# Optimization experiments

Hardware: AMD Instinct MI355X
Metric: run time of the kernel (lower is better)

The kernel has to match this reference:

```python
import jax, jax.numpy as jnp
import numpy as np
from jax import lax

PAD = 1
T, B, V, E, H, K = 256, 64, 50000, 300, 256, 20  # H = hidden_dim//2 per direction


def setup_inputs() -> dict:
    key = jax.random.key(0)
    ks = jax.random.split(key, 14)
    lengths = jnp.sort(jax.random.randint(ks[0], (B,), T // 2, T + 1))[::-1]  # sorted desc like pack_padded
    toks = jax.random.randint(ks[1], (T, B), 2, V)
    tpos = jnp.arange(T)[:, None]
    x = jnp.where(tpos < lengths[None, :], toks, PAD)
    n = jax.random.normal
    s = 1.0 / np.sqrt(H)
    emb = (n(ks[2], (V, E)) * 0.1).at[PAD].set(0.0)  # padding_idx row zeroed
    Wih0 = n(ks[3], (2, 4 * H, E)) * s       # [dir, 4H, in]
    Whh0 = n(ks[4], (2, 4 * H, H)) * s
    b0 = n(ks[5], (2, 4 * H)) * s            # b_ih + b_hh folded together
    Wih1 = n(ks[6], (2, 4 * H, 2 * H)) * s
    Whh1 = n(ks[7], (2, 4 * H, H)) * s
    b1 = n(ks[8], (2, 4 * H)) * s
    W_out = n(ks[9], (K, 2 * H)) * s
    b_out = n(ks[10], (K,)) * s
    trans = n(ks[11], (K, K)) * 0.1
    start = n(ks[12], (K,)) * 0.1
    end = n(ks[13], (K,)) * 0.1
    return dict(x=x, sent_lengths=lengths, emb=emb, Wih0=Wih0, Whh0=Whh0, b0=b0,
                Wih1=Wih1, Whh1=Whh1, b1=b1, W_out=W_out, b_out=b_out,
                trans=trans, start=start, end=end)


def _lstm_dir(xs, m, Wih, Whh, b):
    # xs [T,B,D], m [T,B,1] float mask. PyTorch gate order i,f,g,o.
    xg = jnp.einsum('tbd,gd->tbg', xs, Wih) + b  # big GEMM up-front
    h0 = jnp.zeros((xs.shape[1], H), xs.dtype)

    def step(carry, inp):
        h, c = carry
        g_t, m_t = inp
        gates = g_t + h @ Whh.T
        i, f, g, o = jnp.split(gates, 4, -1)
        c_new = jax.nn.sigmoid(f) * c + jax.nn.sigmoid(i) * jnp.tanh(g)
        h_new = jax.nn.sigmoid(o) * jnp.tanh(c_new)
        # freeze state at padded steps (pack_padded semantics); padded outputs are zero
        return (jnp.where(m_t > 0, h_new, h), jnp.where(m_t > 0, c_new, c)), h_new * m_t

    _, out = lax.scan(step, (h0, h0), (xg, m))
    return out


def _bilstm(xs, m, rev, Wih, Whh, b):
    out_f = _lstm_dir(xs, m, Wih[0], Whh[0], b[0])
    xs_r = jnp.take_along_axis(xs, rev[:, :, None], 0)  # reverse within each length
    out_b = jnp.take_along_axis(_lstm_dir(xs_r, m, Wih[1], Whh[1], b[1]), rev[:, :, None], 0)
    return jnp.concatenate([out_f, out_b], -1)


def reference(x, sent_lengths, emb, Wih0, Whh0, b0, Wih1, Whh1, b1, W_out, b_out, trans, start, end):
    mask = x != PAD                               # [T,B]
    m = mask[:, :, None].astype(emb.dtype)
    tpos = jnp.arange(T)[:, None]
    rev = jnp.where(tpos < sent_lengths[None, :], sent_lengths[None, :] - 1 - tpos, tpos)
    h = emb[x]                                    # [T,B,E]
    h = _bilstm(h, m, rev, Wih0, Whh0, b0)
    h = _bilstm(h, m, rev, Wih1, Whh1, b1)
    emis = jnp.einsum('tbh,kh->tbk', h, W_out) + b_out  # [T,B,K]

    # Viterbi decode (torchcrf semantics)
    score0 = start[None, :] + emis[0]             # [B,K]

    def vstep(sc, inp):
        e_t, m_t = inp
        cand = sc[:, :, None] + trans[None] + e_t[:, None, :]  # [B,prev,next]
        best = cand.max(1)
        ptr = cand.argmax(1).astype(jnp.int32)
        sc2 = jnp.where(m_t[:, None], best, sc)
        # identity pointer at padded steps so backtrace passes tags through
        ptr = jnp.where(m_t[:, None], ptr, jnp.arange(K, dtype=jnp.int32)[None, :])
        return sc2, ptr

    score, hist = lax.scan(vstep, score0, (emis[1:], mask[1:]))
    score = score + end[None, :]                  # score frozen at seq end -> same as adding at last valid step
    last = jnp.argmax(score, -1).astype(jnp.int32)

    def back(tag, ptr):
        prev = jnp.take_along_axis(ptr, tag[:, None], 1)[:, 0]
        return prev, prev

    _, tags_prev = lax.scan(back, last, hist, reverse=True)
    tags = jnp.concatenate([tags_prev, last[None, :]], 0)  # [T,B]
    return jnp.where(mask, tags, 0)
```

## Files before the change

### kernel.cpp

```cpp
#include <hip/hip_runtime.h>
#include <stdint.h>


#define T_ 256
#define B_ 64
#define EPAD 304
#define KTAG 20
#define TB_ (T_ * B_)
#define RES 80
#define NQ 44


__global__ void prep_embed(const int* __restrict__ x, const float* __restrict__ emb,
                           float* __restrict__ xsA) {
  int r = blockIdx.x;
  int tok = x[r];
  const float* src = emb + (size_t)tok * 300;
  for (int e = threadIdx.x; e < EPAD; e += 64)
    xsA[(size_t)r * EPAD + e] = (e < 300) ? src[e] : 0.f;
}

__global__ void prep_b0t(const float* __restrict__ Wih0, float* __restrict__ B0t) {
  int idx = blockIdx.x * 256 + threadIdx.x;
  if (idx >= 2048 * EPAD) return;
  int n = idx / EPAD, k = idx % EPAD;
  B0t[idx] = (k < 300) ? Wih0[(size_t)n * 300 + k] : 0.f;
}

__global__ void prep_bot64(const float* __restrict__ Wout, float* __restrict__ Bot,
                           const float* __restrict__ bout, float* __restrict__ biaso) {
  int idx = blockIdx.x * 256 + threadIdx.x;
  int n = idx >> 9, k = idx & 511;
  Bot[idx] = (n < KTAG) ? Wout[(size_t)n * 512 + k] : 0.f;
  if (idx < 64) biaso[idx] = (idx < KTAG) ? bout[idx] : 0.f;
}

__global__ void prep_whh2(const float* __restrict__ Whh, float* __restrict__ whhL) {
  int idx = blockIdx.x * 256 + threadIdx.x;
  int d = idx >> 18, rem = idx & 262143, k = rem >> 10, tg = rem & 1023;
  int row = (tg & 3) * 256 + (tg >> 2);
  float v = Whh[(size_t)d * 262144 + (size_t)row * 256 + k];
  if (k < RES) whhL[(size_t)(d * RES + k) * 1024 + tg] = v;
  else {
    int kk = k - RES, q = kk >> 2, e = kk & 3;
    whhL[(size_t)2 * RES * 1024 + ((size_t)(d * NQ + q) * 1024 + tg) * 4 + e] = v;
  }
}

__global__ __launch_bounds__(256) void gemm_f32(
    const float* __restrict__ A, int lda, const float* __restrict__ Bt, int ldb,
    float* __restrict__ C, int ldc, const float* __restrict__ bias,
    int ntn, int K) {
  const int tm = blockIdx.x / ntn, tn = blockIdx.x % ntn;
  const int m0 = tm * 64, n0 = tn * 64;
  __shared__ __align__(16) float As[16][64];
  __shared__ __align__(16) float Bs[16][64];
  const int tid = threadIdx.x;
  const int mm = tid >> 2, kq = (tid & 3) * 4;
  const int tx = tid & 15, ty = tid >> 4;
  float acc[4][4] = {};
  for (int k0 = 0; k0 < K; k0 += 16) {
    float4 av = *(const float4*)&A[(size_t)(m0 + mm) * lda + k0 + kq];
    float4 bv = *(const float4*)&Bt[(size_t)(n0 + mm) * ldb + k0 + kq];
    __syncthreads();
    As[kq + 0][mm] = av.x; As[kq + 1][mm] = av.y;
    As[kq + 2][mm] = av.z; As[kq + 3][mm] = av.w;
    Bs[kq + 0][mm] = bv.x; Bs[kq + 1][mm] = bv.y;
    Bs[kq + 2][mm] = bv.z; Bs[kq + 3][mm] = bv.w;
    __syncthreads();
#pragma unroll
    for (int kk = 0; kk < 16; ++kk) {
      float4 a4 = *(const float4*)&As[kk][ty * 4];
      float4 b4 = *(const float4*)&Bs[kk][tx * 4];
      acc[0][0] += a4.x * b4.x; acc[0][1] += a4.x * b4.y;
      acc[0][2] += a4.x * b4.z; acc[0][3] += a4.x * b4.w;
      acc[1][0] += a4.y * b4.x; acc[1][1] += a4.y * b4.y;
      acc[1][2] += a4.y * b4.z; acc[1][3] += a4.y * b4.w;
      acc[2][0] += a4.z * b4.x; acc[2][1] += a4.z * b4.y;
      acc[2][2] += a4.z * b4.z; acc[2][3] += a4.z * b4.w;
      acc[3][0] += a4.w * b4.x; acc[3][1] += a4.w * b4.y;
      acc[3][2] += a4.w * b4.z; acc[3][3] += a4.w * b4.w;
    }
  }
#pragma unroll
  for (int i = 0; i < 4; ++i)
#pragma unroll
    for (int j = 0; j < 4; ++j)
      C[(size_t)(m0 + ty * 4 + i) * ldc + n0 + tx * 4 + j] =
          acc[i][j] + bias[n0 + tx * 4 + j];
}

__global__ __launch_bounds__(1024) void lstm_rec(
    const float* __restrict__ xg, const float* __restrict__ whhL,
    float* __restrict__ out, const int* __restrict__ lens) {
  const int wg = blockIdx.x, dir = wg & 1, b = wg >> 1;
  const int len = lens[b];
  const int tg = threadIdx.x;
  const int j = tg >> 2, gt = tg & 3;
  const int xrow = gt * 256 + j;

  float wres[RES];
#pragma unroll
  for (int p = 0; p < RES; ++p)
    wres[p] = whhL[(size_t)(dir * RES + p) * 1024 + tg];
  const float* sp = whhL + (size_t)2 * RES * 1024 + ((size_t)dir * NQ * 1024 + tg) * 4;

  __shared__ __align__(16) float hsd[2][256];
  if (tg < 256) hsd[0][tg] = 0.f;
  float c = 0.f;
  __syncthreads();

  const int lane = tg & 63, qb = lane & ~3;

  for (int s = 0; s < len; ++s) {
    const int t = dir ? (len - 1 - s) : s;
    const int r = t * B_ + b;
    float xv = xg[(size_t)r * 2048 + dir * 1024 + xrow];
    const float4* Hr = (const float4*)hsd[s & 1];
    float a = 0.f;
#pragma unroll
    for (int p = 0; p < RES / 4; ++p) {
      float4 h4 = Hr[p];
      a += wres[4 * p] * h4.x + wres[4 * p + 1] * h4.y +
           wres[4 * p + 2] * h4.z + wres[4 * p + 3] * h4.w;
    }
#pragma unroll 4
    for (int q = 0; q < NQ; ++q) {
      float4 wv = *(const float4*)(sp + (size_t)q * 4096);
      float4 h4 = Hr[RES / 4 + q];
      a += wv.x * h4.x + wv.y * h4.y + wv.z * h4.z + wv.w * h4.w;
    }
    a += xv;
    float v1 = __shfl(a, qb | 1);
    float v2 = __shfl(a, qb | 2);
    float v3 = __shfl(a, qb | 3);
    if (gt == 0) {
      float si = 1.f / (1.f + expf(-a));
      float sf = 1.f / (1.f + expf(-v1));
      float so = 1.f / (1.f + expf(-v3));
      c = sf * c + si * tanhf(v2);
      float h = so * tanhf(c);
      hsd[(s + 1) & 1][j] = h;
      out[(size_t)r * 512 + dir * 256 + j] = h;
    }
    __syncthreads();
  }
  for (int t = len; t < T_; ++t)
    if (gt == 0) out[(size_t)(t * B_ + b) * 512 + dir * 256 + j] = 0.f;
}

__global__ __launch_bounds__(64) void viterbi(
    const float* __restrict__ emis, const float* __restrict__ trans,
    const float* __restrict__ startv, const float* __restrict__ endv,
    const int* __restrict__ lens, int* __restrict__ outp) {
  int b = blockIdx.x, lane = threadIdx.x;
  __shared__ float tr[KTAG * KTAG];
  __shared__ float fin[KTAG];
  __shared__ unsigned char hist[T_ * KTAG];
  for (int i = lane; i < KTAG * KTAG; i += 64) tr[i] = trans[i];
  int len = lens[b];
  float score = (lane < KTAG) ? startv[lane] + emis[(size_t)b * 64 + lane] : -3e38f;
  __syncthreads();
  for (int t = 1; t < len; ++t) {
    float e = (lane < KTAG) ? emis[(size_t)(t * B_ + b) * 64 + lane] : 0.f;
    float best = -3e38f; int bp = 0;
    for (int p = 0; p < KTAG; ++p) {
      float cand = (__shfl(score, p) + tr[p * KTAG + lane]) + e;
      if (cand > best) { best = cand; bp = p; }
    }
    if (lane < KTAG) { score = best; hist[t * KTAG + lane] = (unsigned char)bp; }
  }
  if (lane < KTAG) fin[lane] = score + endv[lane];
  __syncthreads();
  if (lane == 0) {
    float bb = -3e38f; int tag = 0;
    for (int p = 0; p < KTAG; ++p)
      if (fin[p] > bb) { bb = fin[p]; tag = p; }
    for (int t = len - 1; t >= 1; --t) {
      outp[t * B_ + b] = tag;
      tag = hist[t * KTAG + tag];
    }
    outp[b] = tag;
  }
  for (int t = len + lane; t < T_; t += 64) outp[t * B_ + b] = 0;
}

__global__ void sentinel_fill(int* __restrict__ outp, int val) {
  int i = blockIdx.x * 256 + threadIdx.x;
  if (i < TB_) outp[i] = val;
}
__global__ void diag_init(int* __restrict__ f) { if (threadIdx.x == 0) f[0] = 0; }
__global__ void check_nan(const float* __restrict__ p, long n, int* __restrict__ f) {
  long i0 = (long)blockIdx.x * 256 + threadIdx.x;
  int bad = 0;
  for (long i = i0; i < n; i += (long)gridDim.x * 256)
    if (!(fabsf(p[i]) <= 1e8f)) bad = 1;
  if (bad) atomicOr(&f[0], 1);
}
__global__ void verdict(const int* __restrict__ f, int* __restrict__ outp) {
  if (f[0]) outp[threadIdx.x] = -4096;
}


extern "C" void kernel_launch(void* const* d_in, const int* in_sizes, int n_in,
                              void* d_out, int out_size, void* d_ws, size_t ws_size,
                              hipStream_t stream) {
  int* outp = (int*)d_out;

  static const int exp_sizes[14] = {16384, 64, 15000000, 614400, 524288, 2048,
                                    1048576, 524288, 2048, 10240, 20, 400, 20, 20};
  int badi = (n_in == 14) ? -1 : 14;
  if (badi < 0)
    for (int i = 0; i < 14; ++i)
      if (in_sizes[i] != exp_sizes[i]) { badi = i; break; }
  if (badi >= 0) {
    hipLaunchKernelGGL(sentinel_fill, dim3((TB_ + 255) / 256), dim3(256), 0, stream,
                       outp, -(20000 + badi));
    return;
  }

  const int*   x      = (const int*)d_in[0];
  const int*   lens   = (const int*)d_in[1];
  const float* emb    = (const float*)d_in[2];
  const float* Wih0   = (const float*)d_in[3];
  const float* Whh0   = (const float*)d_in[4];
  const float* b0     = (const float*)d_in[5];
  const float* Wih1   = (const float*)d_in[6];
  const float* Whh1   = (const float*)d_in[7];
  const float* b1     = (const float*)d_in[8];
  const float* Wout   = (const float*)d_in[9];
  const float* bout   = (const float*)d_in[10];
  const float* trans  = (const float*)d_in[11];
  const float* startv = (const float*)d_in[12];
  const float* endv   = (const float*)d_in[13];

  const size_t sz_whh = (size_t)(2 * RES * 1024 + 2 * NQ * 1024 * 4) * 4;

  const size_t need =
      (size_t)TB_ * 2048 * 4
    + (size_t)TB_ * EPAD * 4
    + (size_t)TB_ * 512 * 4
    + (size_t)2048 * EPAD * 4
    + (size_t)64 * 512 * 4
    + 2 * sz_whh
    + 64 * 4
    + (size_t)TB_ * 64 * 4
    + 64;

  if (ws_size < need) {
    hipLaunchKernelGGL(sentinel_fill, dim3((TB_ + 255) / 256), dim3(256), 0, stream,
                       outp, -(int)(10000 + (ws_size >> 20)));
    return;
  }

  char* w = (char*)d_ws;
  float* xg    = (float*)w;  w += (size_t)TB_ * 2048 * 4;
  float* xsA   = (float*)w;  w += (size_t)TB_ * EPAD * 4;
  float* outh  = (float*)w;  w += (size_t)TB_ * 512 * 4;
  float* B0t   = (float*)w;  w += (size_t)2048 * EPAD * 4;
  float* Bot   = (float*)w;  w += (size_t)64 * 512 * 4;
  float* whh0L = (float*)w;  w += sz_whh;
  float* whh1L = (float*)w;  w += sz_whh;
  float* biaso = (float*)w;  w += 64 * 4;
  float* emis  = (float*)w;  w += (size_t)TB_ * 64 * 4;
  int*   diag  = (int*)w;    w += 64;

  hipLaunchKernelGGL(diag_init, dim3(1), dim3(64), 0, stream, diag);
  hipLaunchKernelGGL(prep_embed, dim3(TB_), dim3(64), 0, stream, x, emb, xsA);
  hipLaunchKernelGGL(prep_b0t, dim3((2048 * EPAD + 255) / 256), dim3(256), 0, stream, Wih0, B0t);
  hipLaunchKernelGGL(prep_bot64, dim3(128), dim3(256), 0, stream, Wout, Bot, bout, biaso);
  hipLaunchKernelGGL(prep_whh2, dim3(2048), dim3(256), 0, stream, Whh0, whh0L);
  hipLaunchKernelGGL(prep_whh2, dim3(2048), dim3(256), 0, stream, Whh1, whh1L);

  hipLaunchKernelGGL(gemm_f32, dim3(256 * 32), dim3(256), 0, stream,
                     xsA, EPAD, B0t, EPAD, xg, 2048, b0, 32, EPAD);
  hipLaunchKernelGGL(lstm_rec, dim3(128), dim3(1024), 0, stream, xg, whh0L, outh, lens);
  hipLaunchKernelGGL(gemm_f32, dim3(256 * 32), dim3(256), 0, stream,
                     outh, 512, Wih1, 512, xg, 2048, b1, 32, 512);
  hipLaunchKernelGGL(lstm_rec, dim3(128), dim3(1024), 0, stream, xg, whh1L, outh, lens);
  hipLaunchKernelGGL(gemm_f32, dim3(256), dim3(256), 0, stream,
                     outh, 512, Bot, 512, emis, 64, biaso, 1, 512);
  hipLaunchKernelGGL(check_nan, dim3(256), dim3(256), 0, stream,
                     emis, (long)TB_ * 64, diag);
  hipLaunchKernelGGL(viterbi, dim3(B_), dim3(64), 0, stream,
                     emis, trans, startv, endv, lens, outp);
  hipLaunchKernelGGL(verdict, dim3(1), dim3(64), 0, stream, diag, outp);
}
```

Before: 4.468 ms.

## Split recurrent weights across registers, LDS and streamed global; broadcast h via readlane

Repartitions the recurrent Whh slice per thread into 64 register-resident columns, 12 columns cached in LDS, and 180 columns streamed from global. The hidden state is loaded once per lane as a float4 and broadcast with readlane instead of repeated LDS float4 reads. Accumulation is split into two chains, and launch bounds gain an occupancy hint. This is meant to cut LDS read traffic and register pressure in the serial recurrence, in exchange for more global weight streaming per step.

Measured after the change: 4.778 ms. 7.0% more time.

```diff
diff --git a/kernel.cpp b/kernel.cpp
--- a/kernel.cpp
+++ b/kernel.cpp
@@ -7,8 +7,17 @@
 #define EPAD 304
 #define KTAG 20
 #define TB_ (T_ * B_)
-#define RES 80
-#define NQ 44
+
+#define KR 64
+#define KL 12
+#define KLQ 3
+#define NQS 45
+#define WLDS_OFF (2 * KR * 1024)
+#define WSTR_OFF (WLDS_OFF + 2 * KLQ * 1024 * 4)
+
+__device__ __forceinline__ float rlane(float v, int l) {
+  return __int_as_float(__builtin_amdgcn_readlane(__float_as_int(v), l));
+}
 
 
 __global__ void prep_embed(const int* __restrict__ x, const float* __restrict__ emb,
@@ -40,10 +49,14 @@
   int d = idx >> 18, rem = idx & 262143, k = rem >> 10, tg = rem & 1023;
   int row = (tg & 3) * 256 + (tg >> 2);
   float v = Whh[(size_t)d * 262144 + (size_t)row * 256 + k];
-  if (k < RES) whhL[(size_t)(d * RES + k) * 1024 + tg] = v;
-  else {
-    int kk = k - RES, q = kk >> 2, e = kk & 3;
-    whhL[(size_t)2 * RES * 1024 + ((size_t)(d * NQ + q) * 1024 + tg) * 4 + e] = v;
+  if (k < KR) {
+    whhL[(size_t)(d * KR + k) * 1024 + tg] = v;
+  } else if (k < KR + KL) {
+    int kk = k - KR, q = kk >> 2, e = kk & 3;
+    whhL[WLDS_OFF + (size_t)((d * KLQ + q) * 1024 + tg) * 4 + e] = v;
+  } else {
+    int kk = k - KR - KL, q = kk >> 2, e = kk & 3;
+    whhL[WSTR_OFF + (size_t)((d * NQS + q) * 1024 + tg) * 4 + e] = v;
   }
 }
 
@@ -90,47 +103,67 @@
           acc[i][j] + bias[n0 + tx * 4 + j];
 }
 
-__global__ __launch_bounds__(1024) void lstm_rec(
+__global__ __launch_bounds__(1024, 4) void lstm_rec(
     const float* __restrict__ xg, const float* __restrict__ whhL,
     float* __restrict__ out, const int* __restrict__ lens) {
   const int wg = blockIdx.x, dir = wg & 1, b = wg >> 1;
   const int len = lens[b];
   const int tg = threadIdx.x;
   const int j = tg >> 2, gt = tg & 3;
-  const int xrow = gt * 256 + j;
-
-  float wres[RES];
-#pragma unroll
-  for (int p = 0; p < RES; ++p)
-    wres[p] = whhL[(size_t)(dir * RES + p) * 1024 + tg];
-  const float* sp = whhL + (size_t)2 * RES * 1024 + ((size_t)dir * NQ * 1024 + tg) * 4;
-
+  const int row = gt * 256 + j;
+
+  float wres[KR];
+#pragma unroll
+  for (int k = 0; k < KR; ++k)
+    wres[k] = whhL[(size_t)(dir * KR + k) * 1024 + tg];
+
+  __shared__ __align__(16) float4 wlds[KLQ][1024];
   __shared__ __align__(16) float hsd[2][256];
+#pragma unroll
+  for (int q = 0; q < KLQ; ++q)
+    wlds[q][tg] = *(const float4*)&whhL[WLDS_OFF + (size_t)((dir * KLQ + q) * 1024 + tg) * 4];
   if (tg < 256) hsd[0][tg] = 0.f;
   float c = 0.f;
   __syncthreads();
 
+  const float* sp = whhL + WSTR_OFF + (size_t)dir * NQS * 4096 + (size_t)tg * 4;
+
   const int lane = tg & 63, qb = lane & ~3;
 
   for (int s = 0; s < len; ++s) {
     const int t = dir ? (len - 1 - s) : s;
-    const int r = t * B_ + b;
-    float xv = xg[(size_t)r * 2048 + dir * 1024 + xrow];
-    const float4* Hr = (const float4*)hsd[s & 1];
-    float a = 0.f;
-#pragma unroll
-    for (int p = 0; p < RES / 4; ++p) {
-      float4 h4 = Hr[p];
-      a += wres[4 * p] * h4.x + wres[4 * p + 1] * h4.y +
-           wres[4 * p + 2] * h4.z + wres[4 * p + 3] * h4.w;
-    }
-#pragma unroll 4
-    for (int q = 0; q < NQ; ++q) {
-      float4 wv = *(const float4*)(sp + (size_t)q * 4096);
-      float4 h4 = Hr[RES / 4 + q];
-      a += wv.x * h4.x + wv.y * h4.y + wv.z * h4.z + wv.w * h4.w;
-    }
-    a += xv;
+    const int rp = t * B_ + b;
+    float xv = xg[(size_t)rp * 2048 + dir * 1024 + row];
+    float4 hv = *(const float4*)&hsd[s & 1][lane * 4];
+
+    float acc0 = 0.f, acc1 = 0.f;
+#pragma unroll
+    for (int q = 0; q < KR / 4; ++q) {
+      float b0 = rlane(hv.x, q), b1 = rlane(hv.y, q);
+      float b2 = rlane(hv.z, q), b3 = rlane(hv.w, q);
+      acc0 += wres[4 * q + 0] * b0 + wres[4 * q + 1] * b1;
+      acc1 += wres[4 * q + 2] * b2 + wres[4 * q + 3] * b3;
+    }
+#pragma unroll
+    for (int q3 = 0; q3 < KLQ; ++q3) {
+      int q = KR / 4 + q3;
+      float4 wl = wlds[q3][tg];
+      float b0 = rlane(hv.x, q), b1 = rlane(hv.y, q);
+      float b2 = rlane(hv.z, q), b3 = rlane(hv.w, q);
+      acc0 += wl.x * b0 + wl.y * b1;
+      acc1 += wl.z * b2 + wl.w * b3;
+    }
+#pragma unroll 5
+    for (int qq = 0; qq < NQS; ++qq) {
+      int q = KR / 4 + KLQ + qq;
+      float4 wv = *(const float4*)(sp + (size_t)qq * 4096);
+      float b0 = rlane(hv.x, q), b1 = rlane(hv.y, q);
+      float b2 = rlane(hv.z, q), b3 = rlane(hv.w, q);
+      acc0 += wv.x * b0 + wv.y * b1;
+      acc1 += wv.z * b2 + wv.w * b3;
+    }
+
+    float a = acc0 + acc1 + xv;
     float v1 = __shfl(a, qb | 1);
     float v2 = __shfl(a, qb | 2);
     float v3 = __shfl(a, qb | 3);
@@ -141,7 +174,7 @@
       c = sf * c + si * tanhf(v2);
       float h = so * tanhf(c);
       hsd[(s + 1) & 1][j] = h;
-      out[(size_t)r * 512 + dir * 256 + j] = h;
+      out[(size_t)rp * 512 + dir * 256 + j] = h;
     }
     __syncthreads();
   }
@@ -234,7 +267,7 @@
   const float* startv = (const float*)d_in[12];
   const float* endv   = (const float*)d_in[13];
 
-  const size_t sz_whh = (size_t)(2 * RES * 1024 + 2 * NQ * 1024 * 4) * 4;
+  const size_t sz_whh = (size_t)524288 * 4;
 
   const size_t need =
       (size_t)TB_ * 2048 * 4
```

## Split LSTM recurrence across 4 workgroups per direction with global atomic step sync

Applied to the files above, without the earlier changes.

The recurrent kernel now splits each direction's 256 hidden units across 4 workgroups, and each workgroup handles a pair of batch rows. Hidden state is exchanged through a global double buffer, and steps are synchronised with an agent-scope atomic counter that each block spins on. Weights are relaid out per chunk and streamed from global/L2 as float4, with h broadcast via readlane instead of LDS. A large dummy shared array limits occupancy to one block per CU so all 256 blocks are co-resident. This trades per-step cross-block sync latency for more parallelism and smaller per-block weight slices, and it risks deadlock if the blocks are not all co-resident.

Result: slower. 10.90 ms (+143.9%).

```diff
diff --git a/kernel.cpp b/kernel.cpp
--- a/kernel.cpp
+++ b/kernel.cpp
@@ -7,8 +7,10 @@
 #define EPAD 304
 #define KTAG 20
 #define TB_ (T_ * B_)
-#define RES 80
-#define NQ 44
+
+__device__ __forceinline__ float rlane(float v, int l) {
+  return __int_as_float(__builtin_amdgcn_readlane(__float_as_int(v), l));
+}
 
 
 __global__ void prep_embed(const int* __restrict__ x, const float* __restrict__ emb,
@@ -35,16 +37,21 @@
   if (idx < 64) biaso[idx] = (idx < KTAG) ? bout[idx] : 0.f;
 }
 
-__global__ void prep_whh2(const float* __restrict__ Whh, float* __restrict__ whhL) {
+__global__ void prep_whh3(const float* __restrict__ Whh, float* __restrict__ whhS) {
   int idx = blockIdx.x * 256 + threadIdx.x;
-  int d = idx >> 18, rem = idx & 262143, k = rem >> 10, tg = rem & 1023;
-  int row = (tg & 3) * 256 + (tg >> 2);
+  int d = idx >> 18, rem = idx & 262143, row = rem >> 8, k = rem & 255;
   float v = Whh[(size_t)d * 262144 + (size_t)row * 256 + k];
-  if (k < RES) whhL[(size_t)(d * RES + k) * 1024 + tg] = v;
-  else {
-    int kk = k - RES, q = kk >> 2, e = kk & 3;
-    whhL[(size_t)2 * RES * 1024 + ((size_t)(d * NQ + q) * 1024 + tg) * 4 + e] = v;
-  }
+  int gt = row >> 8, u = row & 255;
+  int chunk = u >> 6, j = u & 63;
+  int rr = j * 4 + gt;
+  int q = k >> 2, e = k & 3;
+  whhS[((((size_t)d * 4 + chunk) * 64 + q) * 256 + rr) * 4 + e] = v;
+}
+
+__global__ void zero_sync(float* __restrict__ Hg, int* __restrict__ ctr) {
+  int i = blockIdx.x * 256 + threadIdx.x;
+  if (i < 32768) Hg[i] = 0.f;
+  else if (i < 32768 + 64) ctr[i - 32768] = 0;
 }
 
 __global__ __launch_bounds__(256) void gemm_f32(
@@ -90,63 +97,79 @@
           acc[i][j] + bias[n0 + tx * 4 + j];
 }
 
-__global__ __launch_bounds__(1024) void lstm_rec(
-    const float* __restrict__ xg, const float* __restrict__ whhL,
-    float* __restrict__ out, const int* __restrict__ lens) {
-  const int wg = blockIdx.x, dir = wg & 1, b = wg >> 1;
+__global__ __launch_bounds__(512) void lstm_rec(
+    const float* __restrict__ xg, const float* __restrict__ whhS,
+    float* __restrict__ out, const int* __restrict__ lens,
+    float* __restrict__ Hg, int* __restrict__ ctr, int* __restrict__ diagf) {
+  __shared__ float occupad[20496];
+  const int blk = blockIdx.x;
+  const int chunk = blk & 3, d = (blk >> 2) & 1, bp = blk >> 3;
+  const int tg = threadIdx.x;
+  const int wv_ = tg >> 6, l = tg & 63;
+  const int b_i = wv_ >> 2, wq = wv_ & 3;
+  const int b = bp * 2 + b_i;
+  const int rr = (wq << 6) | l;
+  const int gt = rr & 3, j = rr >> 2;
+  const int unit = chunk * 64 + j;
+  const int row = gt * 256 + unit;
   const int len = lens[b];
-  const int tg = threadIdx.x;
-  const int j = tg >> 2, gt = tg & 3;
-  const int xrow = gt * 256 + j;
-
-  float wres[RES];
-#pragma unroll
-  for (int p = 0; p < RES; ++p)
-    wres[p] = whhL[(size_t)(dir * RES + p) * 1024 + tg];
-  const float* sp = whhL + (size_t)2 * RES * 1024 + ((size_t)dir * NQ * 1024 + tg) * 4;
-
-  __shared__ __align__(16) float hsd[2][256];
-  if (tg < 256) hsd[0][tg] = 0.f;
+  const int maxlen = lens[bp * 2];
+  if (len == 0x7fffffff) occupad[0] = (float)tg;
+  const float* wbase = whhS + ((size_t)(d * 4 + chunk) << 16);
+  int* myc = ctr + (d * 32 + bp);
+  const int qb = l & ~3;
   float c = 0.f;
-  __syncthreads();
-
-  const int lane = tg & 63, qb = lane & ~3;
-
-  for (int s = 0; s < len; ++s) {
-    const int t = dir ? (len - 1 - s) : s;
-    const int r = t * B_ + b;
-    float xv = xg[(size_t)r * 2048 + dir * 1024 + xrow];
-    const float4* Hr = (const float4*)hsd[s & 1];
-    float a = 0.f;
-#pragma unroll
-    for (int p = 0; p < RES / 4; ++p) {
-      float4 h4 = Hr[p];
-      a += wres[4 * p] * h4.x + wres[4 * p + 1] * h4.y +
-           wres[4 * p + 2] * h4.z + wres[4 * p + 3] * h4.w;
-    }
-#pragma unroll 4
-    for (int q = 0; q < NQ; ++q) {
-      float4 wv = *(const float4*)(sp + (size_t)q * 4096);
-      float4 h4 = Hr[RES / 4 + q];
-      a += wv.x * h4.x + wv.y * h4.y + wv.z * h4.z + wv.w * h4.w;
-    }
-    a += xv;
-    float v1 = __shfl(a, qb | 1);
-    float v2 = __shfl(a, qb | 2);
-    float v3 = __shfl(a, qb | 3);
-    if (gt == 0) {
-      float si = 1.f / (1.f + expf(-a));
-      float sf = 1.f / (1.f + expf(-v1));
-      float so = 1.f / (1.f + expf(-v3));
-      c = sf * c + si * tanhf(v2);
-      float h = so * tanhf(c);
-      hsd[(s + 1) & 1][j] = h;
-      out[(size_t)r * 512 + dir * 256 + j] = h;
+  long polls = 0;
+
+  for (int s = 0; s < maxlen; ++s) {
+    if (tg == 0) {
+      const int tgt = 4 * s;
+      while (__hip_atomic_load(myc, __ATOMIC_ACQUIRE, __HIP_MEMORY_SCOPE_AGENT) < tgt) {
+        __builtin_amdgcn_s_sleep(2);
+        if (++polls > 20000000L) { atomicOr(diagf, 2); break; }
+      }
     }
     __syncthreads();
-  }
-  for (int t = len; t < T_; ++t)
-    if (gt == 0) out[(size_t)(t * B_ + b) * 512 + dir * 256 + j] = 0.f;
+    const float* hsrc = Hg + (((size_t)(s & 1) * 2 + d) * 64 + b) * 256;
+    float* hdst = Hg + (((size_t)((s + 1) & 1) * 2 + d) * 64 + b) * 256;
+    if (s < len) {
+      const int t = d ? (len - 1 - s) : s;
+      const float xv = xg[(size_t)(t * B_ + b) * 2048 + d * 1024 + row];
+      float4 hv = *(const float4*)&hsrc[l * 4];
+      float acc0 = 0.f, acc1 = 0.f;
+#pragma unroll 8
+      for (int q = 0; q < 64; ++q) {
+        float4 wvq = *(const float4*)(wbase + (((size_t)q << 8) + rr) * 4);
+        float b0 = rlane(hv.x, q), b1 = rlane(hv.y, q);
+        float b2 = rlane(hv.z, q), b3 = rlane(hv.w, q);
+        acc0 += wvq.x * b0 + wvq.y * b1;
+        acc1 += wvq.z * b2 + wvq.w * b3;
+      }
+      float a = acc0 + acc1 + xv;
+      float v1 = __shfl(a, qb | 1);
+      float v2 = __shfl(a, qb | 2);
+      float v3 = __shfl(a, qb | 3);
+      if (gt == 0) {
+        float si = 1.f / (1.f + expf(-a));
+        float sf = 1.f / (1.f + expf(-v1));
+        float so = 1.f / (1.f + expf(-v3));
+        c = sf * c + si * tanhf(v2);
+        float h = so * tanhf(c);
+        hdst[unit] = h;
+        out[(size_t)(t * B_ + b) * 512 + d * 256 + unit] = h;
+      }
+    } else {
+      if (gt == 0) hdst[unit] = hsrc[unit];
+    }
+    __syncthreads();
+    if (tg == 0) {
+      __threadfence();
+      __hip_atomic_fetch_add(myc, 1, __ATOMIC_RELEASE, __HIP_MEMORY_SCOPE_AGENT);
+    }
+  }
+  if (gt == 0)
+    for (int t = len; t < T_; ++t)
+      out[(size_t)(t * B_ + b) * 512 + d * 256 + unit] = 0.f;
 }
 
 __global__ __launch_bounds__(64) void viterbi(
@@ -234,7 +257,7 @@
   const float* startv = (const float*)d_in[12];
   const float* endv   = (const float*)d_in[13];
 
-  const size_t sz_whh = (size_t)(2 * RES * 1024 + 2 * NQ * 1024 * 4) * 4;
+  const size_t sz_whh = (size_t)524288 * 4;
 
   const size_t need =
       (size_t)TB_ * 2048 * 4
@@ -245,6 +268,8 @@
     + 2 * sz_whh
     + 64 * 4
     + (size_t)TB_ * 64 * 4
+    + (size_t)65536 * 4
+    + 64 * 4
     + 64;
 
   if (ws_size < need) {
@@ -259,25 +284,31 @@
   float* outh  = (float*)w;  w += (size_t)TB_ * 512 * 4;
   float* B0t   = (float*)w;  w += (size_t)2048 * EPAD * 4;
   float* Bot   = (float*)w;  w += (size_t)64 * 512 * 4;
-  float* whh0L = (float*)w;  w += sz_whh;
-  float* whh1L = (float*)w;  w += sz_whh;
+  float* whh0S = (float*)w;  w += sz_whh;
+  float* whh1S = (float*)w;  w += sz_whh;
   float* biaso = (float*)w;  w += 64 * 4;
   float* emis  = (float*)w;  w += (size_t)TB_ * 64 * 4;
+  float* Hg    = (float*)w;  w += (size_t)65536 * 4;
+  int*   ctr   = (int*)w;    w += 64 * 4;
   int*   diag  = (int*)w;    w += 64;
 
   hipLaunchKernelGGL(diag_init, dim3(1), dim3(64), 0, stream, diag);
   hipLaunchKernelGGL(prep_embed, dim3(TB_), dim3(64), 0, stream, x, emb, xsA);
   hipLaunchKernelGGL(prep_b0t, dim3((2048 * EPAD + 255) / 256), dim3(256), 0, stream, Wih0, B0t);
   hipLaunchKernelGGL(prep_bot64, dim3(128), dim3(256), 0, stream, Wout, Bot, bout, biaso);
-  hipLaunchKernelGGL(prep_whh2, dim3(2048), dim3(256), 0, stream, Whh0, whh0L);
-  hipLaunchKernelGGL(prep_whh2, dim3(2048), dim3(256), 0, stream, Whh1, whh1L);
+  hipLaunchKernelGGL(prep_whh3, dim3(2048), dim3(256), 0, stream, Whh0, whh0S);
+  hipLaunchKernelGGL(prep_whh3, dim3(2048), dim3(256), 0, stream, Whh1, whh1S);
 
   hipLaunchKernelGGL(gemm_f32, dim3(256 * 32), dim3(256), 0, stream,
                      xsA, EPAD, B0t, EPAD, xg, 2048, b0, 32, EPAD);
-  hipLaunchKernelGGL(lstm_rec, dim3(128), dim3(1024), 0, stream, xg, whh0L, outh, lens);
+  hipLaunchKernelGGL(zero_sync, dim3(129), dim3(256), 0, stream, Hg, ctr);
+  hipLaunchKernelGGL(lstm_rec, dim3(256), dim3(512), 0, stream,
+                     xg, whh0S, outh, lens, Hg, ctr, diag);
   hipLaunchKernelGGL(gemm_f32, dim3(256 * 32), dim3(256), 0, stream,
                      outh, 512, Wih1, 512, xg, 2048, b1, 32, 512);
-  hipLaunchKernelGGL(lstm_rec, dim3(128), dim3(1024), 0, stream, xg, whh1L, outh, lens);
+  hipLaunchKernelGGL(zero_sync, dim3(129), dim3(256), 0, stream, Hg, ctr);
+  hipLaunchKernelGGL(lstm_rec, dim3(256), dim3(512), 0, stream,
+                     xg, whh1S, outh, lens, Hg, ctr, diag);
   hipLaunchKernelGGL(gemm_f32, dim3(256), dim3(256), 0, stream,
                      outh, 512, Bot, 512, emis, 64, biaso, 1, 512);
   hipLaunchKernelGGL(check_nan, dim3(256), dim3(256), 0, stream,
```
